# Performance work log

Measured on AMD Instinct MI355X. Metric: run time of the kernel, lower is better.

Reference implementation:

```python
import jax, jax.numpy as jnp
import numpy as np


def _chamfer(src, tgt):
    # src: [B, N, 3], tgt: [B, M, 3]
    x2 = jnp.sum(src * src, axis=-1)              # [B, N]
    y2 = jnp.sum(tgt * tgt, axis=-1)              # [B, M]
    xy = jnp.einsum('bnd,bmd->bnm', src, tgt)     # [B, N, M]
    d2 = x2[:, :, None] + y2[:, None, :] - 2.0 * xy
    d2 = jnp.maximum(d2, 0.0)                     # guard tiny negatives
    cham_x = jnp.min(d2, axis=2)                  # [B, N] min over tgt
    cham_y = jnp.min(d2, axis=1)                  # [B, M] min over src
    # point_reduction='mean', batch_reduction='sum'
    loss = jnp.sum(jnp.mean(cham_x, axis=1)) + jnp.sum(jnp.mean(cham_y, axis=1))
    return loss


def setup_inputs() -> dict:
    key = jax.random.key(0)
    k1, k2 = jax.random.split(key)
    src = jax.random.normal(k1, (16, 4096, 3), dtype=jnp.float32)
    tgt = jax.random.normal(k2, (16, 4096, 3), dtype=jnp.float32)
    return {"src": src, "tgt": tgt}


def reference(src, tgt):
    wgeo = 1.0
    return wgeo * _chamfer(src, tgt)
```

## Files before the change

### kernel.cpp

```cpp
#include <hip/hip_runtime.h>
#include <hip/hip_bf16.h>


#define BATCH   16
#define NPTS    4096
#define CHUNKC  512
#define NCHUNKS (NPTS / CHUNKC)
#define NSTRIPS 16

typedef __attribute__((ext_vector_type(8)))  short short8;
typedef __attribute__((ext_vector_type(16))) float float16;

union U4S8 { uint4 u; short8 s; };

__device__ inline unsigned int bfb(float v) {
    __hip_bfloat16 h = __float2bfloat16(v);
    unsigned short u; __builtin_memcpy(&u, &h, 2);
    return (unsigned int)u;
}
__device__ inline float bff(float v) { return __bfloat162float(__float2bfloat16(v)); }

#define ONEB 0x3F80u

__device__ inline void buildA(float x, float y, float z, uint4& w0, uint4& w1) {
    float xhf = bff(x), yhf = bff(y), zhf = bff(z);
    float f = fmaf(x, x, fmaf(y, y, z * z));
    float fhf = bff(f);
    unsigned xh = bfb(xhf), yh = bfb(yhf), zh = bfb(zhf);
    unsigned xl = bfb(x - xhf), yl = bfb(y - yhf), zl = bfb(z - zhf);
    unsigned fh = bfb(fhf), fl = bfb(f - fhf);
    w0 = make_uint4(xh | (yh << 16), zh | (xh << 16),
                    yh | (zh << 16), xl | (yl << 16));
    w1 = make_uint4(zl | (fh << 16), fl | (ONEB << 16), ONEB, 0u);
}

__device__ inline void buildB(float x, float y, float z, uint4& w0, uint4& w1) {
    float xhf = bff(x), yhf = bff(y), zhf = bff(z);
    float f = fmaf(x, x, fmaf(y, y, z * z));
    float fhf = bff(f);
    unsigned a = bfb(-2.0f * xhf), b = bfb(-2.0f * yhf), c = bfb(-2.0f * zhf);
    unsigned d = bfb(-2.0f * (x - xhf)), e = bfb(-2.0f * (y - yhf)),
             g = bfb(-2.0f * (z - zhf));
    unsigned fh = bfb(fhf), fl = bfb(f - fhf);
    w0 = make_uint4(a | (b << 16), c | (d << 16),
                    e | (g << 16), a | (b << 16));
    w1 = make_uint4(c | (ONEB << 16), ONEB | (fh << 16), fl, 0u);
}

__global__ __launch_bounds__(256, 2) void chamfer_fused_kernel(
    const float* __restrict__ src, const float* __restrict__ tgt,
    float* __restrict__ out)
{
    __shared__ uint4 sbuf[2][2][CHUNKC];
    __shared__ float wsum[4];

    int blk = blockIdx.x;
    const int strip = blk & (NSTRIPS - 1); blk >>= 4;
    const int b     = blk & 15;            blk >>= 4;
    const int dir   = blk;

    const int lane = threadIdx.x & 63;
    const int w    = threadIdx.x >> 6;
    const int half = lane >> 5;
    const int l5   = lane & 31;

    const float* Araw = (dir ? tgt : src) + (size_t)b * NPTS * 3;
    const float* Braw = (dir ? src : tgt) + (size_t)b * NPTS * 3;

    short8 afr[2];
#pragma unroll
    for (int g = 0; g < 2; g++) {
        int row = strip * 256 + g * 128 + w * 32 + l5;
        uint4 w0, w1;
        buildA(Araw[3 * row], Araw[3 * row + 1], Araw[3 * row + 2], w0, w1);
        U4S8 t; t.u = half ? w1 : w0;
        afr[g] = t.s;
    }

    auto convert = [&](int c, int bi) {
#pragma unroll
        for (int k = 0; k < 2; k++) {
            int lp = (int)threadIdx.x + k * 256;
            int p  = c * CHUNKC + lp;
            uint4 w0, w1;
            buildB(Braw[3 * p], Braw[3 * p + 1], Braw[3 * p + 2], w0, w1);
            sbuf[bi][0][lp] = w0;
            sbuf[bi][1][lp] = w1;
        }
    };

    const float16 z16 = {0.f,0.f,0.f,0.f,0.f,0.f,0.f,0.f,
                         0.f,0.f,0.f,0.f,0.f,0.f,0.f,0.f};
    float rm[2][16];
#pragma unroll
    for (int g = 0; g < 2; g++)
#pragma unroll
        for (int r = 0; r < 16; r++) rm[g][r] = 1e30f;

    convert(0, 0);
    for (int c = 0; c < NCHUNKS; c++) {
        __syncthreads();
        if (c + 1 < NCHUNKS) convert(c + 1, (c + 1) & 1);
        const int bi = c & 1;
#pragma unroll 2
        for (int j2 = 0; j2 < CHUNKC / 64; j2++) {
            U4S8 t0, t1;
            t0.u = sbuf[bi][half][j2 * 64 + l5];
            t1.u = sbuf[bi][half][j2 * 64 + 32 + l5];
            float16 a00 = __builtin_amdgcn_mfma_f32_32x32x16_bf16(afr[0], t0.s, z16, 0, 0, 0);
            float16 a01 = __builtin_amdgcn_mfma_f32_32x32x16_bf16(afr[0], t1.s, z16, 0, 0, 0);
            float16 a10 = __builtin_amdgcn_mfma_f32_32x32x16_bf16(afr[1], t0.s, z16, 0, 0, 0);
            float16 a11 = __builtin_amdgcn_mfma_f32_32x32x16_bf16(afr[1], t1.s, z16, 0, 0, 0);
#pragma unroll
            for (int r = 0; r < 16; r++) {
                rm[0][r] = fminf(fminf(a00[r], a01[r]), rm[0][r]);
                rm[1][r] = fminf(fminf(a10[r], a11[r]), rm[1][r]);
            }
        }
    }

#pragma unroll
    for (int mask = 1; mask <= 16; mask <<= 1)
#pragma unroll
        for (int g = 0; g < 2; g++)
#pragma unroll
            for (int r = 0; r < 16; r++)
                rm[g][r] = fminf(rm[g][r], __shfl_xor(rm[g][r], mask, 64));

    float s = 0.0f;
#pragma unroll
    for (int g = 0; g < 2; g++)
#pragma unroll
        for (int r = 0; r < 16; r++) s += fmaxf(rm[g][r], 0.0f);
    s += __shfl_xor(s, 32, 64);

    if (lane == 0) wsum[w] = s;
    __syncthreads();
    if (threadIdx.x == 0)
        atomicAdd(out, (wsum[0] + wsum[1] + wsum[2] + wsum[3]) * (1.0f / (float)NPTS));
}

extern "C" void kernel_launch(void* const* d_in, const int* in_sizes, int n_in,
                              void* d_out, int out_size, void* d_ws, size_t ws_size,
                              hipStream_t stream)
{
    const float* src = (const float*)d_in[0];
    const float* tgt = (const float*)d_in[1];
    float* out = (float*)d_out;

    hipMemsetAsync(out, 0, sizeof(float), stream);
    chamfer_fused_kernel<<<2 * BATCH * NSTRIPS, 256, 0, stream>>>(src, tgt, out);
}
```

Measured before the change: 79.71 us.

## Split column range across two blocks with atomicMin row minima and reduce kernel

Each block now covers only half of the target columns, which doubles the grid to 1024 blocks, and launch bounds are raised to 4 blocks per CU. Per-row minima are merged across the two column halves with atomicMin on float bits in a workspace buffer, and a second kernel sums them into the output. The global loads for the next chunk are now issued before the MFMA loop and converted to LDS afterwards, to hide load latency. The cost is an extra memset, a second kernel launch, and atomic traffic.

```diff
diff --git a/kernel.cpp b/kernel.cpp
--- a/kernel.cpp
+++ b/kernel.cpp
@@ -5,8 +5,10 @@
 #define BATCH   16
 #define NPTS    4096
 #define CHUNKC  512
-#define NCHUNKS (NPTS / CHUNKC)
+#define COLSPB  2048
+#define NCHUNKS (COLSPB / CHUNKC)
 #define NSTRIPS 16
+#define NMINS   (2 * BATCH * NPTS)
 
 typedef __attribute__((ext_vector_type(8)))  short short8;
 typedef __attribute__((ext_vector_type(16))) float float16;
@@ -47,14 +49,14 @@
     w1 = make_uint4(c | (ONEB << 16), ONEB | (fh << 16), fl, 0u);
 }
 
-__global__ __launch_bounds__(256, 2) void chamfer_fused_kernel(
+__global__ __launch_bounds__(256, 4) void chamfer_mfma_kernel(
     const float* __restrict__ src, const float* __restrict__ tgt,
-    float* __restrict__ out)
+    unsigned int* __restrict__ mins)
 {
     __shared__ uint4 sbuf[2][2][CHUNKC];
-    __shared__ float wsum[4];
 
     int blk = blockIdx.x;
+    const int ch    = blk & 1;             blk >>= 1;
     const int strip = blk & (NSTRIPS - 1); blk >>= 4;
     const int b     = blk & 15;            blk >>= 4;
     const int dir   = blk;
@@ -66,6 +68,7 @@
 
     const float* Araw = (dir ? tgt : src) + (size_t)b * NPTS * 3;
     const float* Braw = (dir ? src : tgt) + (size_t)b * NPTS * 3;
+    const int colbase = ch * COLSPB;
 
     short8 afr[2];
 #pragma unroll
@@ -77,13 +80,22 @@
         afr[g] = t.s;
     }
 
-    auto convert = [&](int c, int bi) {
+    float nx[2][3];
+    auto loadRaw = [&](int c) {
+#pragma unroll
+        for (int k = 0; k < 2; k++) {
+            int p = colbase + c * CHUNKC + (int)threadIdx.x + k * 256;
+            nx[k][0] = Braw[3 * p + 0];
+            nx[k][1] = Braw[3 * p + 1];
+            nx[k][2] = Braw[3 * p + 2];
+        }
+    };
+    auto convertWrite = [&](int bi) {
 #pragma unroll
         for (int k = 0; k < 2; k++) {
             int lp = (int)threadIdx.x + k * 256;
-            int p  = c * CHUNKC + lp;
             uint4 w0, w1;
-            buildB(Braw[3 * p], Braw[3 * p + 1], Braw[3 * p + 2], w0, w1);
+            buildB(nx[k][0], nx[k][1], nx[k][2], w0, w1);
             sbuf[bi][0][lp] = w0;
             sbuf[bi][1][lp] = w1;
         }
@@ -97,26 +109,27 @@
 #pragma unroll
         for (int r = 0; r < 16; r++) rm[g][r] = 1e30f;
 
-    convert(0, 0);
+    loadRaw(0);
+    convertWrite(0);
     for (int c = 0; c < NCHUNKS; c++) {
         __syncthreads();
-        if (c + 1 < NCHUNKS) convert(c + 1, (c + 1) & 1);
+        if (c + 1 < NCHUNKS) loadRaw(c + 1);
         const int bi = c & 1;
 #pragma unroll 2
         for (int j2 = 0; j2 < CHUNKC / 64; j2++) {
             U4S8 t0, t1;
             t0.u = sbuf[bi][half][j2 * 64 + l5];
             t1.u = sbuf[bi][half][j2 * 64 + 32 + l5];
-            float16 a00 = __builtin_amdgcn_mfma_f32_32x32x16_bf16(afr[0], t0.s, z16, 0, 0, 0);
-            float16 a01 = __builtin_amdgcn_mfma_f32_32x32x16_bf16(afr[0], t1.s, z16, 0, 0, 0);
-            float16 a10 = __builtin_amdgcn_mfma_f32_32x32x16_bf16(afr[1], t0.s, z16, 0, 0, 0);
-            float16 a11 = __builtin_amdgcn_mfma_f32_32x32x16_bf16(afr[1], t1.s, z16, 0, 0, 0);
 #pragma unroll
-            for (int r = 0; r < 16; r++) {
-                rm[0][r] = fminf(fminf(a00[r], a01[r]), rm[0][r]);
-                rm[1][r] = fminf(fminf(a10[r], a11[r]), rm[1][r]);
+            for (int g = 0; g < 2; g++) {
+                float16 a0 = __builtin_amdgcn_mfma_f32_32x32x16_bf16(afr[g], t0.s, z16, 0, 0, 0);
+                float16 a1 = __builtin_amdgcn_mfma_f32_32x32x16_bf16(afr[g], t1.s, z16, 0, 0, 0);
+#pragma unroll
+                for (int r = 0; r < 16; r++)
+                    rm[g][r] = fminf(fminf(a0[r], a1[r]), rm[g][r]);
             }
         }
+        if (c + 1 < NCHUNKS) convertWrite((c + 1) & 1);
     }
 
 #pragma unroll
@@ -127,17 +140,38 @@
             for (int r = 0; r < 16; r++)
                 rm[g][r] = fminf(rm[g][r], __shfl_xor(rm[g][r], mask, 64));
 
+    if (l5 == 0) {
+        unsigned int* mrow = mins + (size_t)(dir * BATCH + b) * NPTS;
+#pragma unroll
+        for (int g = 0; g < 2; g++)
+#pragma unroll
+            for (int r = 0; r < 16; r++) {
+                int row = strip * 256 + g * 128 + w * 32 + (r & 3) + 8 * (r >> 2) + 4 * half;
+                float v = fmaxf(rm[g][r], 0.0f);
+                atomicMin(&mrow[row], __float_as_uint(v));
+            }
+    }
+}
+
+__global__ __launch_bounds__(256) void chamfer_reduce_kernel(
+    const unsigned int* __restrict__ mins, float* __restrict__ out)
+{
     float s = 0.0f;
+    for (int idx = blockIdx.x * blockDim.x + threadIdx.x; idx < NMINS;
+         idx += gridDim.x * blockDim.x) {
+        s += __uint_as_float(mins[idx]);
+    }
 #pragma unroll
-    for (int g = 0; g < 2; g++)
-#pragma unroll
-        for (int r = 0; r < 16; r++) s += fmaxf(rm[g][r], 0.0f);
-    s += __shfl_xor(s, 32, 64);
-
+    for (int off = 32; off > 0; off >>= 1) s += __shfl_down(s, off, 64);
+    __shared__ float wsum[4];
+    int lane = threadIdx.x & 63;
+    int w = threadIdx.x >> 6;
     if (lane == 0) wsum[w] = s;
     __syncthreads();
-    if (threadIdx.x == 0)
-        atomicAdd(out, (wsum[0] + wsum[1] + wsum[2] + wsum[3]) * (1.0f / (float)NPTS));
+    if (threadIdx.x == 0) {
+        float tot = wsum[0] + wsum[1] + wsum[2] + wsum[3];
+        atomicAdd(out, tot * (1.0f / (float)NPTS));
+    }
 }
 
 extern "C" void kernel_launch(void* const* d_in, const int* in_sizes, int n_in,
@@ -147,7 +181,11 @@
     const float* src = (const float*)d_in[0];
     const float* tgt = (const float*)d_in[1];
     float* out = (float*)d_out;
+    unsigned int* mins = (unsigned int*)d_ws;
 
+    hipMemsetAsync(mins, 0xFF, (size_t)NMINS * sizeof(unsigned int), stream);
     hipMemsetAsync(out, 0, sizeof(float), stream);
-    chamfer_fused_kernel<<<2 * BATCH * NSTRIPS, 256, 0, stream>>>(src, tgt, out);
+
+    chamfer_mfma_kernel<<<2 * BATCH * NSTRIPS * 2, 256, 0, stream>>>(src, tgt, mins);
+    chamfer_reduce_kernel<<<128, 256, 0, stream>>>(mins, out);
 }
```

After: 83.84 us. +5.2%, slower.

## Halve rows per block, raise occupancy, and prefetch next chunk across MFMA loop

Applied to the files above, without the earlier changes.

Each block now handles 128 A rows instead of 256, so the grid doubles to 1024 blocks, and launch bounds ask for 4 blocks per SIMD group to raise occupancy. The next chunk's raw B points are loaded into registers before the MFMA loop and converted and written to LDS after it, to hide global load latency behind compute. The cost is that each staged B chunk is reused by half as many A rows, so LDS conversion and global reads per MFMA roughly double.

```diff
diff --git a/kernel.cpp b/kernel.cpp
--- a/kernel.cpp
+++ b/kernel.cpp
@@ -6,7 +6,7 @@
 #define NPTS    4096
 #define CHUNKC  512
 #define NCHUNKS (NPTS / CHUNKC)
-#define NSTRIPS 16
+#define NSTRIPS 32
 
 typedef __attribute__((ext_vector_type(8)))  short short8;
 typedef __attribute__((ext_vector_type(16))) float float16;
@@ -47,7 +47,7 @@
     w1 = make_uint4(c | (ONEB << 16), ONEB | (fh << 16), fl, 0u);
 }
 
-__global__ __launch_bounds__(256, 2) void chamfer_fused_kernel(
+__global__ __launch_bounds__(256, 4) void chamfer_kernel(
     const float* __restrict__ src, const float* __restrict__ tgt,
     float* __restrict__ out)
 {
@@ -55,35 +55,44 @@
     __shared__ float wsum[4];
 
     int blk = blockIdx.x;
-    const int strip = blk & (NSTRIPS - 1); blk >>= 4;
+    const int strip = blk & (NSTRIPS - 1); blk >>= 5;
     const int b     = blk & 15;            blk >>= 4;
     const int dir   = blk;
 
-    const int lane = threadIdx.x & 63;
-    const int w    = threadIdx.x >> 6;
+    const int t    = threadIdx.x;
+    const int lane = t & 63;
+    const int w    = t >> 6;
     const int half = lane >> 5;
     const int l5   = lane & 31;
 
     const float* Araw = (dir ? tgt : src) + (size_t)b * NPTS * 3;
     const float* Braw = (dir ? src : tgt) + (size_t)b * NPTS * 3;
 
-    short8 afr[2];
-#pragma unroll
-    for (int g = 0; g < 2; g++) {
-        int row = strip * 256 + g * 128 + w * 32 + l5;
+    short8 afr;
+    {
+        int row = strip * 128 + w * 32 + l5;
         uint4 w0, w1;
         buildA(Araw[3 * row], Araw[3 * row + 1], Araw[3 * row + 2], w0, w1);
-        U4S8 t; t.u = half ? w1 : w0;
-        afr[g] = t.s;
+        U4S8 tt; tt.u = half ? w1 : w0;
+        afr = tt.s;
     }
 
-    auto convert = [&](int c, int bi) {
+    float nx[2][3];
+    auto loadRaw = [&](int c) {
 #pragma unroll
         for (int k = 0; k < 2; k++) {
-            int lp = (int)threadIdx.x + k * 256;
-            int p  = c * CHUNKC + lp;
+            int p = c * CHUNKC + t + k * 256;
+            nx[k][0] = Braw[3 * p + 0];
+            nx[k][1] = Braw[3 * p + 1];
+            nx[k][2] = Braw[3 * p + 2];
+        }
+    };
+    auto convertWrite = [&](int bi) {
+#pragma unroll
+        for (int k = 0; k < 2; k++) {
+            int lp = t + k * 256;
             uint4 w0, w1;
-            buildB(Braw[3 * p], Braw[3 * p + 1], Braw[3 * p + 2], w0, w1);
+            buildB(nx[k][0], nx[k][1], nx[k][2], w0, w1);
             sbuf[bi][0][lp] = w0;
             sbuf[bi][1][lp] = w1;
         }
@@ -91,52 +100,44 @@
 
     const float16 z16 = {0.f,0.f,0.f,0.f,0.f,0.f,0.f,0.f,
                          0.f,0.f,0.f,0.f,0.f,0.f,0.f,0.f};
-    float rm[2][16];
+    float rm[16];
 #pragma unroll
-    for (int g = 0; g < 2; g++)
-#pragma unroll
-        for (int r = 0; r < 16; r++) rm[g][r] = 1e30f;
+    for (int r = 0; r < 16; r++) rm[r] = 1e30f;
 
-    convert(0, 0);
+    loadRaw(0);
+    convertWrite(0);
     for (int c = 0; c < NCHUNKS; c++) {
         __syncthreads();
-        if (c + 1 < NCHUNKS) convert(c + 1, (c + 1) & 1);
+        if (c + 1 < NCHUNKS) loadRaw(c + 1);
         const int bi = c & 1;
 #pragma unroll 2
         for (int j2 = 0; j2 < CHUNKC / 64; j2++) {
             U4S8 t0, t1;
             t0.u = sbuf[bi][half][j2 * 64 + l5];
             t1.u = sbuf[bi][half][j2 * 64 + 32 + l5];
-            float16 a00 = __builtin_amdgcn_mfma_f32_32x32x16_bf16(afr[0], t0.s, z16, 0, 0, 0);
-            float16 a01 = __builtin_amdgcn_mfma_f32_32x32x16_bf16(afr[0], t1.s, z16, 0, 0, 0);
-            float16 a10 = __builtin_amdgcn_mfma_f32_32x32x16_bf16(afr[1], t0.s, z16, 0, 0, 0);
-            float16 a11 = __builtin_amdgcn_mfma_f32_32x32x16_bf16(afr[1], t1.s, z16, 0, 0, 0);
+            float16 a0 = __builtin_amdgcn_mfma_f32_32x32x16_bf16(afr, t0.s, z16, 0, 0, 0);
+            float16 a1 = __builtin_amdgcn_mfma_f32_32x32x16_bf16(afr, t1.s, z16, 0, 0, 0);
 #pragma unroll
-            for (int r = 0; r < 16; r++) {
-                rm[0][r] = fminf(fminf(a00[r], a01[r]), rm[0][r]);
-                rm[1][r] = fminf(fminf(a10[r], a11[r]), rm[1][r]);
-            }
+            for (int r = 0; r < 16; r++)
+                rm[r] = fminf(fminf(a0[r], a1[r]), rm[r]);
         }
+        if (c + 1 < NCHUNKS) convertWrite((c + 1) & 1);
     }
 
 #pragma unroll
     for (int mask = 1; mask <= 16; mask <<= 1)
 #pragma unroll
-        for (int g = 0; g < 2; g++)
-#pragma unroll
-            for (int r = 0; r < 16; r++)
-                rm[g][r] = fminf(rm[g][r], __shfl_xor(rm[g][r], mask, 64));
+        for (int r = 0; r < 16; r++)
+            rm[r] = fminf(rm[r], __shfl_xor(rm[r], mask, 64));
 
     float s = 0.0f;
 #pragma unroll
-    for (int g = 0; g < 2; g++)
-#pragma unroll
-        for (int r = 0; r < 16; r++) s += fmaxf(rm[g][r], 0.0f);
+    for (int r = 0; r < 16; r++) s += fmaxf(rm[r], 0.0f);
     s += __shfl_xor(s, 32, 64);
 
     if (lane == 0) wsum[w] = s;
     __syncthreads();
-    if (threadIdx.x == 0)
+    if (t == 0)
         atomicAdd(out, (wsum[0] + wsum[1] + wsum[2] + wsum[3]) * (1.0f / (float)NPTS));
 }
 
@@ -149,5 +150,5 @@
     float* out = (float*)d_out;
 
     hipMemsetAsync(out, 0, sizeof(float), stream);
-    chamfer_fused_kernel<<<2 * BATCH * NSTRIPS, 256, 0, stream>>>(src, tgt, out);
+    chamfer_kernel<<<2 * BATCH * NSTRIPS, 256, 0, stream>>>(src, tgt, out);
 }
```

New measurement: 81.46 us. 2.2% more time.
